# Performance work log

Hardware: AMD Instinct MI355X
Metric: run time of the kernel (lower is better)

The kernel has to match this reference:

```python
import jax, jax.numpy as jnp
import numpy as np

PC_RANGE = (-51.2, -51.2, -5.0, 51.2, 51.2, 3.0)
IMG_H, IMG_W = 256.0, 704.0
EPS = 1e-5


def conv2d(x, w, b, pad):
    y = jax.lax.conv_general_dilated(x, w, (1, 1), ((pad, pad), (pad, pad)),
                                     dimension_numbers=('NCHW', 'OIHW', 'NCHW'))
    return y + b[None, :, None, None]


def bilinear_sample(feat, grid):
    # torch.F.grid_sample, bilinear, zeros padding, align_corners=False
    # feat (BN,C,H,W), grid (BN,Q,D,2) in [-1,1] -> (BN,C,Q,D)
    BN, C, H, W = feat.shape
    ix = (grid[..., 0] + 1.0) * (W * 0.5) - 0.5
    iy = (grid[..., 1] + 1.0) * (H * 0.5) - 0.5
    x0 = jnp.floor(ix); y0 = jnp.floor(iy)
    x1 = x0 + 1.0; y1 = y0 + 1.0
    wx1 = ix - x0; wx0 = 1.0 - wx1
    wy1 = iy - y0; wy0 = 1.0 - wy1

    def corner(f, xi, yi):
        inb = ((xi >= 0) & (xi < W) & (yi >= 0) & (yi < H)).astype(f.dtype)
        xc = jnp.clip(xi, 0, W - 1).astype(jnp.int32)
        yc = jnp.clip(yi, 0, H - 1).astype(jnp.int32)
        idx = (yc * W + xc).reshape(-1)
        v = f.reshape(C, H * W)[:, idx].reshape((C,) + xi.shape)
        return v * inb[None]

    def sample_one(f, x0b, y0b, x1b, y1b, w00, w01, w10, w11):
        return (corner(f, x0b, y0b) * w00[None] + corner(f, x1b, y0b) * w01[None]
                + corner(f, x0b, y1b) * w10[None] + corner(f, x1b, y1b) * w11[None])

    return jax.vmap(sample_one)(feat, x0, y0, x1, y1,
                                wx0 * wy0, wx1 * wy0, wx0 * wy1, wx1 * wy1)


def ihr_forward(feat, bev_queries, bev_pos, reference_points, lidar2img, img_aug,
                w_pos, b_pos, w_attn, b_attn, w_out, b_out,
                conv_w, conv_b, bn_gamma, bn_beta, bn_mean, bn_var,
                se_w, se_b, cbam_w, cbam_b, bev_h, bev_w):
    B, Q, C = bev_queries.shape
    N = lidar2img.shape[1]
    q = bev_queries + bev_pos
    off = q @ w_pos + b_pos                                   # (B,Q,1) height offset
    # only_use_height: z <- sigmoid(inverse_sigmoid(z) + off)
    z = jnp.clip(reference_points[..., 2:3], 0.0, 1.0)
    z = jnp.log(jnp.clip(z, EPS, None) / jnp.clip(1.0 - z, EPS, None))
    z = jax.nn.sigmoid(z + off[:, None])                      # (B,D,Q,1)
    rp = jnp.concatenate([reference_points[..., :2], z], -1)  # updated ref points

    # --- feature_sampling ---
    xyz = jnp.stack([
        rp[..., 0] * (PC_RANGE[3] - PC_RANGE[0]) + PC_RANGE[0],
        rp[..., 1] * (PC_RANGE[4] - PC_RANGE[1]) + PC_RANGE[1],
        rp[..., 2] * (PC_RANGE[5] - PC_RANGE[2]) + PC_RANGE[2]], -1)  # (B,D,Q,3)
    pts = jnp.concatenate([xyz, jnp.ones_like(xyz[..., :1])], -1)
    pts = jnp.transpose(pts, (1, 0, 2, 3))                    # (D,B,Q,4)
    D = pts.shape[0]
    cam = jnp.einsum('bnij,dbqj->dbnqi', lidar2img, pts)       # (D,B,N,Q,3)
    depth = cam[..., 2:3]
    mask = depth > EPS
    cam4 = jnp.concatenate([cam[..., :2] / jnp.maximum(depth, EPS), depth,
                            jnp.ones_like(depth)], -1)
    cam2 = jnp.einsum('bnij,dbnqj->dbnqi', img_aug, cam4)[..., :2]
    cam2 = cam2 / jnp.array([IMG_W, IMG_H], cam2.dtype)
    cam2 = (cam2 - 0.5) * 2.0
    mask = (mask & (cam2[..., 0:1] > -1.0) & (cam2[..., 0:1] < 1.0)
            & (cam2[..., 1:2] > -1.0) & (cam2[..., 1:2] < 1.0))
    bev_mask = jnp.nan_to_num(jnp.transpose(mask, (1, 4, 3, 2, 0)).astype(feat.dtype))  # (B,1,Q,N,D)
    grid = jnp.transpose(cam2, (1, 2, 3, 0, 4)).reshape(B * N, Q, D, 2)
    samp = bilinear_sample(feat, grid)                         # (BN,C,Q,D)
    samp = samp.reshape(B, N, C, Q, D).transpose(0, 2, 3, 1, 4)  # (B,C,Q,N,D)
    samp = jnp.nan_to_num(samp)

    attn = jax.nn.sigmoid(q @ w_attn + b_attn).reshape(B, 1, Q, N, 1) * bev_mask
    out = (samp * attn).sum(axis=(3, 4))                       # (B,C,Q)  (D==1)
    out = out.transpose(0, 2, 1) @ w_out + b_out + bev_queries  # (B,Q,C)

    # --- vtransform: Conv3x3 -> BN(eval) -> ReLU -> SE -> CBAM(spatial) ---
    x = out.transpose(0, 2, 1).reshape(B, C, bev_h, bev_w)
    x = conv2d(x, conv_w, conv_b, 1)
    inv = jax.lax.rsqrt(bn_var + 1e-5)
    x = bn_gamma[None, :, None, None] * (x - bn_mean[None, :, None, None]) * inv[None, :, None, None] + bn_beta[None, :, None, None]
    x = jax.nn.relu(x)
    s = jax.nn.sigmoid(x.mean(axis=(2, 3)) @ se_w + se_b)      # SE: GAP + 1x1 conv
    x = x * s[:, :, None, None]
    mx = x.max(axis=1, keepdims=True)
    av = x.mean(axis=1, keepdims=True)
    a = jax.nn.sigmoid(conv2d(jnp.concatenate([mx, av], 1), cbam_w, cbam_b, 3))
    x = x * a
    out = x.reshape(B, C, bev_h * bev_w).transpose(0, 2, 1)
    return out, rp


def setup_inputs() -> dict:
    key = jax.random.key(0)
    ks = jax.random.split(key, 16)
    B, N, C, Q, D = 1, 6, 256, 128 * 128, 1
    H, W = 32, 88
    return {
        'feat': jax.random.normal(ks[0], (B * N, C, H, W), jnp.float32),
        'bev_queries': jax.random.normal(ks[1], (B, Q, C), jnp.float32),
        'bev_pos': jax.random.normal(ks[2], (B, Q, C), jnp.float32),
        'reference_points': jax.random.uniform(ks[3], (B, D, Q, 3), jnp.float32),
        'lidar2img': jax.random.normal(ks[4], (B, N, 3, 4), jnp.float32),
        'img_aug': jax.random.normal(ks[5], (B, N, 3, 4), jnp.float32),
        'w_pos': jax.random.normal(ks[6], (C, 1), jnp.float32) * 0.02,
        'b_pos': jnp.zeros((1,), jnp.float32),
        'w_attn': jax.random.normal(ks[7], (C, N), jnp.float32) * 0.02,
        'b_attn': jnp.zeros((N,), jnp.float32),
        'w_out': jax.random.normal(ks[8], (C, C), jnp.float32) * 0.02,
        'b_out': jnp.zeros((C,), jnp.float32),
        'conv_w': jax.random.normal(ks[9], (C, C, 3, 3), jnp.float32) * 0.02,
        'conv_b': jnp.zeros((C,), jnp.float32),
        'bn_gamma': jnp.ones((C,), jnp.float32),
        'bn_beta': jnp.zeros((C,), jnp.float32),
        'bn_mean': jnp.zeros((C,), jnp.float32),
        'bn_var': jax.random.uniform(ks[10], (C,), jnp.float32, 0.5, 1.5),
        'se_w': jax.random.normal(ks[11], (C, C), jnp.float32) * 0.02,
        'se_b': jnp.zeros((C,), jnp.float32),
        'cbam_w': jax.random.normal(ks[12], (1, 2, 7, 7), jnp.float32) * 0.1,
        'cbam_b': jnp.zeros((1,), jnp.float32),
        'bev_h': 128,
        'bev_w': 128,
    }


def reference(feat, bev_queries, bev_pos, reference_points, lidar2img, img_aug,
              w_pos, b_pos, w_attn, b_attn, w_out, b_out,
              conv_w, conv_b, bn_gamma, bn_beta, bn_mean, bn_var,
              se_w, se_b, cbam_w, cbam_b, bev_h, bev_w):
    return ihr_forward(feat, bev_queries, bev_pos, reference_points, lidar2img, img_aug,
                       w_pos, b_pos, w_attn, b_attn, w_out, b_out,
                       conv_w, conv_b, bn_gamma, bn_beta, bn_mean, bn_var,
                       se_w, se_b, cbam_w, cbam_b, bev_h, bev_w)
```

## Files before the change

### kernel.cpp

```cpp
#include <hip/hip_runtime.h>

typedef float  f32x4 __attribute__((ext_vector_type(4)));
typedef short  s16x8 __attribute__((ext_vector_type(8)));
typedef short  s16x4 __attribute__((ext_vector_type(4)));

__device__ __forceinline__ float bf2f(short h) {
    union { unsigned u; float f; } v; v.u = ((unsigned)(unsigned short)h) << 16; return v.f;
}
__device__ __forceinline__ short f2bf(float f) {
    union { float f; unsigned u; } v; v.f = f;
    unsigned r = v.u + 0x7FFFu + ((v.u >> 16) & 1u);
    return (short)(r >> 16);
}
__device__ __forceinline__ float sigf(float x) { return 1.f / (1.f + __expf(-x)); }


__global__ __launch_bounds__(256) void k_prep(
    const float* __restrict__ feat, const float* __restrict__ w_out,
    const float* __restrict__ conv_w, short* __restrict__ featT,
    short* __restrict__ woT, short* __restrict__ w9,
    short* __restrict__ Xp, float* __restrict__ chan_sums)
{
    __shared__ float tile[64][65];
    int b = blockIdx.x, t = threadIdx.x;
    if (b < 2340) {
        ((f32x4*)Xp)[b * 256 + t] = (f32x4){0.f, 0.f, 0.f, 0.f};
    } else if (b < 3396) {
        int bb = b - 2340;
        int n = bb / 176, r = bb % 176, ct = r / 44, ht = r % 44;
        int ty = t >> 6, tx = t & 63;
        const float* src = feat + (n * 256 + ct * 64) * 2816 + ht * 64;
        #pragma unroll
        for (int i = 0; i < 16; ++i) {
            int cl = ty * 16 + i;
            tile[cl][tx] = src[cl * 2816 + tx];
        }
        __syncthreads();
        short* dst = featT + (n * 2816 + ht * 64) * 256 + ct * 64;
        #pragma unroll
        for (int i = 0; i < 16; ++i) {
            int row = ty * 16 + i;
            dst[row * 256 + tx] = f2bf(tile[tx][row]);
        }
    } else if (b < 3652) {
        int idx = (b - 3396) * 256 + t;
        int j = idx >> 8, c = idx & 255;
        woT[j * 256 + c] = f2bf(w_out[c * 256 + j]);
    } else if (b < 3908) {
        int oc = (b - 3652) * 256 + t;
        const float* src = conv_w + oc * 9;
        #pragma unroll
        for (int k = 0; k < 9; ++k) w9[k * 65536 + oc] = f2bf(src[k]);
    } else {
        if (t < 256) chan_sums[t] = 0.f;
    }
}

__global__ __launch_bounds__(256) void k_sample(
    const float* __restrict__ bev_q, const float* __restrict__ bev_pos,
    const float* __restrict__ refp, const float* __restrict__ l2i,
    const float* __restrict__ aug, const float* __restrict__ w_pos,
    const float* __restrict__ b_pos, const float* __restrict__ w_attn,
    const float* __restrict__ b_attn, const short* __restrict__ featT,
    short* __restrict__ S, float* __restrict__ rp_out)
{
    int lane = threadIdx.x & 63;
    int qi = blockIdx.x * 4 + (threadIdx.x >> 6);

    f32x4 qv = *(const f32x4*)(bev_q + qi * 256 + lane * 4);
    {
        f32x4 pv = *(const f32x4*)(bev_pos + qi * 256 + lane * 4);
        qv[0] += pv[0]; qv[1] += pv[1]; qv[2] += pv[2]; qv[3] += pv[3];
    }
    f32x4 wp = *(const f32x4*)(w_pos + lane * 4);
    float op = qv[0]*wp[0] + qv[1]*wp[1] + qv[2]*wp[2] + qv[3]*wp[3];

    float la[6] = {0.f,0.f,0.f,0.f,0.f,0.f};
    const float* wa = w_attn + lane * 24;
    #pragma unroll
    for (int i = 0; i < 4; ++i) {
        #pragma unroll
        for (int n = 0; n < 6; ++n) la[n] += qv[i] * wa[i * 6 + n];
    }
    #pragma unroll
    for (int m = 1; m < 64; m <<= 1) {
        op += __shfl_xor(op, m);
        #pragma unroll
        for (int n = 0; n < 6; ++n) la[n] += __shfl_xor(la[n], m);
    }
    float off = op + b_pos[0];
    float attn[6];
    #pragma unroll
    for (int n = 0; n < 6; ++n) attn[n] = sigf(la[n] + b_attn[n]);

    float rx = refp[qi * 3 + 0], ry = refp[qi * 3 + 1], rz = refp[qi * 3 + 2];
    float zc = fminf(fmaxf(rz, 0.f), 1.f);
    float lg = logf(fmaxf(zc, 1e-5f) / fmaxf(1.f - zc, 1e-5f));
    float zn = sigf(lg + off);
    if (lane == 0) {
        rp_out[qi * 3 + 0] = rx;
        rp_out[qi * 3 + 1] = ry;
        rp_out[qi * 3 + 2] = zn;
    }

    float X = rx * 102.4f - 51.2f;
    float Yc = ry * 102.4f - 51.2f;
    float Z = zn * 8.f - 5.f;

    f32x4 acc = {0.f, 0.f, 0.f, 0.f};
    auto corner = [&](int n, int xi, int yi, float w) {
        if (xi >= 0 && xi < 88 && yi >= 0 && yi < 32) {
            s16x4 v = *(const s16x4*)(featT + (((n * 32 + yi) * 88 + xi) << 8) + (lane << 2));
            acc[0] += w * bf2f(v[0]); acc[1] += w * bf2f(v[1]);
            acc[2] += w * bf2f(v[2]); acc[3] += w * bf2f(v[3]);
        }
    };
    for (int n = 0; n < 6; ++n) {
        const float* L = l2i + n * 12;
        float cx = L[0]*X + L[1]*Yc + L[2]*Z  + L[3];
        float cy = L[4]*X + L[5]*Yc + L[6]*Z  + L[7];
        float d  = L[8]*X + L[9]*Yc + L[10]*Z + L[11];
        float dd = fmaxf(d, 1e-5f);
        float ux = cx / dd, uy = cy / dd;
        const float* A = aug + n * 12;
        float ax = A[0]*ux + A[1]*uy + A[2]*d + A[3];
        float ay = A[4]*ux + A[5]*uy + A[6]*d + A[7];
        float gx = (ax * (1.f / 704.f) - 0.5f) * 2.f;
        float gy = (ay * (1.f / 256.f) - 0.5f) * 2.f;
        bool m = (d > 1e-5f) && (gx > -1.f) && (gx < 1.f) && (gy > -1.f) && (gy < 1.f);
        if (m) {
            float ix = (gx + 1.f) * 44.f - 0.5f;
            float iy = (gy + 1.f) * 16.f - 0.5f;
            float x0f = floorf(ix), y0f = floorf(iy);
            float wx1 = ix - x0f, wx0 = 1.f - wx1;
            float wy1 = iy - y0f, wy0 = 1.f - wy1;
            int x0 = (int)x0f, y0 = (int)y0f, x1 = x0 + 1, y1 = y0 + 1;
            float wn = attn[n];
            corner(n, x0, y0, wn * wx0 * wy0);
            corner(n, x1, y0, wn * wx1 * wy0);
            corner(n, x0, y1, wn * wx0 * wy1);
            corner(n, x1, y1, wn * wx1 * wy1);
        }
    }
    s16x4 sv;
    sv[0] = f2bf(acc[0]); sv[1] = f2bf(acc[1]);
    sv[2] = f2bf(acc[2]); sv[3] = f2bf(acc[3]);
    *(s16x4*)(S + qi * 256 + lane * 4) = sv;
}

__global__ __launch_bounds__(256) void k_gemm(
    const short* __restrict__ S, const short* __restrict__ woT,
    const float* __restrict__ b_out, const float* __restrict__ bev_q,
    short* __restrict__ Xp)
{
    int tid = threadIdx.x, wave = tid >> 6, lane = tid & 63;
    int l15 = lane & 15, quad = lane >> 4;
    int p0 = blockIdx.x * 64, n0 = wave * 64;
    f32x4 acc[4][4];
    #pragma unroll
    for (int mt = 0; mt < 4; ++mt)
        #pragma unroll
        for (int nt = 0; nt < 4; ++nt) acc[mt][nt] = (f32x4){0.f,0.f,0.f,0.f};

    const short* Ab = S   + (p0 + l15) * 256 + quad * 8;
    const short* Bb = woT + (n0 + l15) * 256 + quad * 8;
    #pragma unroll
    for (int kb = 0; kb < 8; ++kb) {
        s16x8 a[4], b[4];
        #pragma unroll
        for (int mt = 0; mt < 4; ++mt) a[mt] = *(const s16x8*)(Ab + mt * 4096 + kb * 32);
        #pragma unroll
        for (int nt = 0; nt < 4; ++nt) b[nt] = *(const s16x8*)(Bb + nt * 4096 + kb * 32);
        #pragma unroll
        for (int mt = 0; mt < 4; ++mt)
            #pragma unroll
            for (int nt = 0; nt < 4; ++nt)
                acc[mt][nt] = __builtin_amdgcn_mfma_f32_16x16x32_bf16(a[mt], b[nt], acc[mt][nt], 0, 0, 0);
    }
    #pragma unroll
    for (int nt = 0; nt < 4; ++nt) {
        int j = n0 + nt * 16 + l15;
        float bo = b_out[j];
        #pragma unroll
        for (int mt = 0; mt < 4; ++mt) {
            #pragma unroll
            for (int r = 0; r < 4; ++r) {
                int p = p0 + mt * 16 + quad * 4 + r;
                float v = acc[mt][nt][r] + bo + bev_q[p * 256 + j];
                int h = p >> 7, w = p & 127;
                Xp[((h + 1) * 144 + (w + 1)) * 256 + j] = f2bf(v);
            }
        }
    }
}

__global__ __launch_bounds__(256) void k_conv(
    const short* __restrict__ Xp, const short* __restrict__ w9,
    const float* __restrict__ conv_b, const float* __restrict__ gamma,
    const float* __restrict__ beta, const float* __restrict__ mean,
    const float* __restrict__ var, short* __restrict__ Y)
{
    int tid = threadIdx.x, wave = tid >> 6, lane = tid & 63;
    int l15 = lane & 15, quad = lane >> 4;
    int p0 = blockIdx.x * 64;
    int h = p0 >> 7, w0 = p0 & 127;
    int m0 = wave * 64;
    f32x4 acc[4][4];
    #pragma unroll
    for (int mt = 0; mt < 4; ++mt)
        #pragma unroll
        for (int nt = 0; nt < 4; ++nt) acc[mt][nt] = (f32x4){0.f,0.f,0.f,0.f};

    const short* Ab0 = w9 + (m0 + l15) * 256 + quad * 8;
    for (int kh = 0; kh < 3; ++kh) {
        for (int kw = 0; kw < 3; ++kw) {
            const short* Ab = Ab0 + (kh * 3 + kw) * 65536;
            const short* Bb = Xp + ((h + kh) * 144 + (w0 + kw + l15)) * 256 + quad * 8;
            #pragma unroll
            for (int kb = 0; kb < 8; ++kb) {
                s16x8 a[4], b[4];
                #pragma unroll
                for (int mt = 0; mt < 4; ++mt) a[mt] = *(const s16x8*)(Ab + mt * 4096 + kb * 32);
                #pragma unroll
                for (int nt = 0; nt < 4; ++nt) b[nt] = *(const s16x8*)(Bb + nt * 4096 + kb * 32);
                #pragma unroll
                for (int mt = 0; mt < 4; ++mt)
                    #pragma unroll
                    for (int nt = 0; nt < 4; ++nt)
                        acc[mt][nt] = __builtin_amdgcn_mfma_f32_16x16x32_bf16(a[mt], b[nt], acc[mt][nt], 0, 0, 0);
            }
        }
    }
    #pragma unroll
    for (int mt = 0; mt < 4; ++mt) {
        #pragma unroll
        for (int r = 0; r < 4; ++r) {
            int o = m0 + mt * 16 + quad * 4 + r;
            float cb = conv_b[o], g = gamma[o], be = beta[o], mu = mean[o];
            float inv = rsqrtf(var[o] + 1e-5f);
            #pragma unroll
            for (int nt = 0; nt < 4; ++nt) {
                int p = p0 + nt * 16 + l15;
                float v = acc[mt][nt][r] + cb;
                v = g * (v - mu) * inv + be;
                v = fmaxf(v, 0.f);
                Y[p * 256 + o] = f2bf(v);
            }
        }
    }
}

__global__ __launch_bounds__(256) void k_csum(const short* __restrict__ Y, float* __restrict__ chan_sums)
{
    int c = threadIdx.x, p0 = blockIdx.x * 64;
    float s = 0.f;
    for (int i = 0; i < 64; ++i) s += bf2f(Y[(p0 + i) * 256 + c]);
    atomicAdd(chan_sums + c, s);
}

__global__ __launch_bounds__(256) void k_se(
    const float* __restrict__ chan_sums, const float* __restrict__ se_w,
    const float* __restrict__ se_b, float* __restrict__ sbuf)
{
    __shared__ float m[256];
    int t = threadIdx.x;
    m[t] = chan_sums[t] * (1.f / 16384.f);
    __syncthreads();
    float a = 0.f;
    for (int c = 0; c < 256; ++c) a += m[c] * se_w[c * 256 + t];
    sbuf[t] = sigf(a + se_b[t]);
}

__global__ __launch_bounds__(256) void k_mxav(
    const short* __restrict__ Y, const float* __restrict__ sbuf,
    float* __restrict__ mx, float* __restrict__ av)
{
    int lane = threadIdx.x & 63;
    int p = blockIdx.x * 4 + (threadIdx.x >> 6);
    f32x4 sv = *(const f32x4*)(sbuf + lane * 4);
    s16x4 yv = *(const s16x4*)(Y + p * 256 + lane * 4);
    float v0 = bf2f(yv[0]) * sv[0], v1 = bf2f(yv[1]) * sv[1];
    float v2 = bf2f(yv[2]) * sv[2], v3 = bf2f(yv[3]) * sv[3];
    float mval = fmaxf(fmaxf(v0, v1), fmaxf(v2, v3));
    float aval = v0 + v1 + v2 + v3;
    #pragma unroll
    for (int m = 1; m < 64; m <<= 1) {
        mval = fmaxf(mval, __shfl_xor(mval, m));
        aval += __shfl_xor(aval, m);
    }
    if (lane == 0) { mx[p] = mval; av[p] = aval * (1.f / 256.f); }
}

__global__ __launch_bounds__(256) void k_cbam(
    const float* __restrict__ mx, const float* __restrict__ av,
    const float* __restrict__ cw, const float* __restrict__ cb,
    float* __restrict__ amap)
{
    int p = blockIdx.x * 256 + threadIdx.x;
    int h = p >> 7, w = p & 127;
    float acc = cb[0];
    for (int kh = 0; kh < 7; ++kh) {
        int yy = h + kh - 3;
        if ((unsigned)yy >= 128u) continue;
        for (int kw = 0; kw < 7; ++kw) {
            int xx = w + kw - 3;
            if ((unsigned)xx >= 128u) continue;
            int q = yy * 128 + xx;
            acc += cw[kh * 7 + kw] * mx[q] + cw[49 + kh * 7 + kw] * av[q];
        }
    }
    amap[p] = sigf(acc);
}

__global__ __launch_bounds__(256) void k_final(
    const short* __restrict__ Y, const float* __restrict__ sbuf,
    const float* __restrict__ amap, float* __restrict__ out0)
{
    int lane = threadIdx.x & 63;
    int p = blockIdx.x * 4 + (threadIdx.x >> 6);
    float a = amap[p];
    f32x4 sv = *(const f32x4*)(sbuf + lane * 4);
    s16x4 yv = *(const s16x4*)(Y + p * 256 + lane * 4);
    f32x4 o;
    o[0] = bf2f(yv[0]) * sv[0] * a;
    o[1] = bf2f(yv[1]) * sv[1] * a;
    o[2] = bf2f(yv[2]) * sv[2] * a;
    o[3] = bf2f(yv[3]) * sv[3] * a;
    *(f32x4*)(out0 + p * 256 + lane * 4) = o;
}

extern "C" void kernel_launch(void* const* d_in, const int* in_sizes, int n_in,
                              void* d_out, int out_size, void* d_ws, size_t ws_size,
                              hipStream_t stream) {
    const float* feat     = (const float*)d_in[0];
    const float* bev_q    = (const float*)d_in[1];
    const float* bev_pos  = (const float*)d_in[2];
    const float* refp     = (const float*)d_in[3];
    const float* l2i      = (const float*)d_in[4];
    const float* aug      = (const float*)d_in[5];
    const float* w_pos    = (const float*)d_in[6];
    const float* b_pos    = (const float*)d_in[7];
    const float* w_attn   = (const float*)d_in[8];
    const float* b_attn   = (const float*)d_in[9];
    const float* w_out    = (const float*)d_in[10];
    const float* b_out    = (const float*)d_in[11];
    const float* conv_w   = (const float*)d_in[12];
    const float* conv_b   = (const float*)d_in[13];
    const float* bn_g     = (const float*)d_in[14];
    const float* bn_b     = (const float*)d_in[15];
    const float* bn_m     = (const float*)d_in[16];
    const float* bn_v     = (const float*)d_in[17];
    const float* se_w     = (const float*)d_in[18];
    const float* se_b     = (const float*)d_in[19];
    const float* cbam_w   = (const float*)d_in[20];
    const float* cbam_b   = (const float*)d_in[21];

    char* ws = (char*)d_ws;
    short* featT     = (short*)(ws + 0);
    short* Ybuf      = (short*)(ws + 0);
    short* Sbuf      = (short*)(ws + 8650752);
    short* Xp        = (short*)(ws + 17039360);
    short* w9        = (short*)(ws + 26624000);
    short* woT       = (short*)(ws + 27803648);
    float* chan_sums = (float*)(ws + 27934720);
    float* sbuf      = (float*)(ws + 27935744);
    float* mx        = (float*)(ws + 27936768);
    float* av        = (float*)(ws + 28002304);
    float* amap      = (float*)(ws + 28067840);

    float* out0   = (float*)d_out;
    float* rp_out = out0 + 16384 * 256;

    hipLaunchKernelGGL(k_prep, dim3(3909), dim3(256), 0, stream,
                       feat, w_out, conv_w, featT, woT, w9, Xp, chan_sums);
    hipLaunchKernelGGL(k_sample, dim3(4096), dim3(256), 0, stream,
                       bev_q, bev_pos, refp, l2i, aug, w_pos, b_pos, w_attn, b_attn,
                       featT, Sbuf, rp_out);
    hipLaunchKernelGGL(k_gemm, dim3(256), dim3(256), 0, stream,
                       Sbuf, woT, b_out, bev_q, Xp);
    hipLaunchKernelGGL(k_conv, dim3(256), dim3(256), 0, stream,
                       Xp, w9, conv_b, bn_g, bn_b, bn_m, bn_v, Ybuf);
    hipLaunchKernelGGL(k_csum, dim3(256), dim3(256), 0, stream, Ybuf, chan_sums);
    hipLaunchKernelGGL(k_se, dim3(1), dim3(256), 0, stream, chan_sums, se_w, se_b, sbuf);
    hipLaunchKernelGGL(k_mxav, dim3(4096), dim3(256), 0, stream, Ybuf, sbuf, mx, av);
    hipLaunchKernelGGL(k_cbam, dim3(64), dim3(256), 0, stream, mx, av, cbam_w, cbam_b, amap);
    hipLaunchKernelGGL(k_final, dim3(4096), dim3(256), 0, stream, Ybuf, sbuf, amap, out0);
}
```

Measured before the change: 274.7 us.

## Stage conv tiles in LDS via global_load_lds and split output channels across blocks

The 3x3 conv kernel used to read weight and activation fragments straight from global memory into registers, one 256-output-channel tile per block. It now copies 64x64 weight and pixel tiles into shared memory with async global-to-LDS loads, then runs MFMA from LDS. Each block now handles only a quarter of the output channels, giving 1024 blocks of 128 threads instead of 256 blocks. This adds parallelism and coalesced loads, but adds two barriers per K-chunk with no double buffering, and each activation tile is now loaded four times (once per channel quarter).

```diff
diff --git a/kernel.cpp b/kernel.cpp
--- a/kernel.cpp
+++ b/kernel.cpp
@@ -13,6 +13,13 @@
     return (short)(r >> 16);
 }
 __device__ __forceinline__ float sigf(float x) { return 1.f / (1.f + __expf(-x)); }
+
+__device__ __forceinline__ void gll16(const void* g, void* l) {
+    __builtin_amdgcn_global_load_lds(
+        (const __attribute__((address_space(1))) unsigned int*)(uintptr_t)g,
+        (__attribute__((address_space(3))) unsigned int*)(uintptr_t)l,
+        16, 0, 0);
+}
 
 
 __global__ __launch_bounds__(256) void k_prep(
@@ -194,57 +201,79 @@
     }
 }
 
-__global__ __launch_bounds__(256) void k_conv(
+__global__ __launch_bounds__(128) void k_conv(
     const short* __restrict__ Xp, const short* __restrict__ w9,
     const float* __restrict__ conv_b, const float* __restrict__ gamma,
     const float* __restrict__ beta, const float* __restrict__ mean,
     const float* __restrict__ var, short* __restrict__ Y)
 {
+    __shared__ short lA[4096];
+    __shared__ short lB[4096];
+
     int tid = threadIdx.x, wave = tid >> 6, lane = tid & 63;
     int l15 = lane & 15, quad = lane >> 4;
-    int p0 = blockIdx.x * 64;
+    int pxt = blockIdx.x >> 2, ocq = blockIdx.x & 3;
+    int p0 = pxt * 64;
     int h = p0 >> 7, w0 = p0 & 127;
-    int m0 = wave * 64;
-    f32x4 acc[4][4];
-    #pragma unroll
-    for (int mt = 0; mt < 4; ++mt)
+    int ocb = ocq * 64;
+
+    f32x4 acc[2][4];
+    #pragma unroll
+    for (int mt = 0; mt < 2; ++mt)
         #pragma unroll
         for (int nt = 0; nt < 4; ++nt) acc[mt][nt] = (f32x4){0.f,0.f,0.f,0.f};
 
-    const short* Ab0 = w9 + (m0 + l15) * 256 + quad * 8;
     for (int kh = 0; kh < 3; ++kh) {
         for (int kw = 0; kw < 3; ++kw) {
-            const short* Ab = Ab0 + (kh * 3 + kw) * 65536;
-            const short* Bb = Xp + ((h + kh) * 144 + (w0 + kw + l15)) * 256 + quad * 8;
-            #pragma unroll
-            for (int kb = 0; kb < 8; ++kb) {
-                s16x8 a[4], b[4];
+            const short* wsrc = w9 + ((kh * 3 + kw) << 16) + (ocb << 8);
+            const short* xsrc = Xp + ((h + kh) * 144 + (w0 + kw)) * 256;
+            for (int cb = 0; cb < 4; ++cb) {
+                int c0 = cb << 6;
                 #pragma unroll
-                for (int mt = 0; mt < 4; ++mt) a[mt] = *(const s16x8*)(Ab + mt * 4096 + kb * 32);
+                for (int j = 0; j < 4; ++j) {
+                    int ia = wave * 256 + j * 64 + lane;
+                    int cg = ia >> 6, ocl = ia & 63;
+                    gll16(wsrc + ocl * 256 + c0 + cg * 8, &lA[ia * 8]);
+                }
                 #pragma unroll
-                for (int nt = 0; nt < 4; ++nt) b[nt] = *(const s16x8*)(Bb + nt * 4096 + kb * 32);
+                for (int j = 0; j < 4; ++j) {
+                    int ib = wave * 256 + j * 64 + lane;
+                    int cg = ib >> 6, px = ib & 63;
+                    gll16(xsrc + px * 256 + c0 + cg * 8, &lB[ib * 8]);
+                }
+                __syncthreads();
                 #pragma unroll
-                for (int mt = 0; mt < 4; ++mt)
+                for (int s = 0; s < 2; ++s) {
+                    int cg = s * 4 + quad;
+                    s16x8 a[2], b[4];
+                    a[0] = *(const s16x8*)&lA[cg * 512 + (wave * 32 + l15) * 8];
+                    a[1] = *(const s16x8*)&lA[cg * 512 + (wave * 32 + 16 + l15) * 8];
                     #pragma unroll
                     for (int nt = 0; nt < 4; ++nt)
-                        acc[mt][nt] = __builtin_amdgcn_mfma_f32_16x16x32_bf16(a[mt], b[nt], acc[mt][nt], 0, 0, 0);
+                        b[nt] = *(const s16x8*)&lB[cg * 512 + (nt * 16 + l15) * 8];
+                    #pragma unroll
+                    for (int mt = 0; mt < 2; ++mt)
+                        #pragma unroll
+                        for (int nt = 0; nt < 4; ++nt)
+                            acc[mt][nt] = __builtin_amdgcn_mfma_f32_16x16x32_bf16(a[mt], b[nt], acc[mt][nt], 0, 0, 0);
+                }
+                __syncthreads();
             }
         }
     }
     #pragma unroll
-    for (int mt = 0; mt < 4; ++mt) {
+    for (int mt = 0; mt < 2; ++mt) {
         #pragma unroll
         for (int r = 0; r < 4; ++r) {
-            int o = m0 + mt * 16 + quad * 4 + r;
-            float cb = conv_b[o], g = gamma[o], be = beta[o], mu = mean[o];
+            int o = ocb + wave * 32 + mt * 16 + quad * 4 + r;
+            float cb_ = conv_b[o], g = gamma[o], be = beta[o], mu = mean[o];
             float inv = rsqrtf(var[o] + 1e-5f);
             #pragma unroll
             for (int nt = 0; nt < 4; ++nt) {
                 int p = p0 + nt * 16 + l15;
-                float v = acc[mt][nt][r] + cb;
+                float v = acc[mt][nt][r] + cb_;
                 v = g * (v - mu) * inv + be;
-                v = fmaxf(v, 0.f);
-                Y[p * 256 + o] = f2bf(v);
+                Y[p * 256 + o] = f2bf(fmaxf(v, 0.f));
             }
         }
     }
@@ -378,7 +407,7 @@
                        featT, Sbuf, rp_out);
     hipLaunchKernelGGL(k_gemm, dim3(256), dim3(256), 0, stream,
                        Sbuf, woT, b_out, bev_q, Xp);
-    hipLaunchKernelGGL(k_conv, dim3(256), dim3(256), 0, stream,
+    hipLaunchKernelGGL(k_conv, dim3(1024), dim3(128), 0, stream,
                        Xp, w9, conv_b, bn_g, bn_b, bn_m, bn_v, Ybuf);
     hipLaunchKernelGGL(k_csum, dim3(256), dim3(256), 0, stream, Ybuf, chan_sums);
     hipLaunchKernelGGL(k_se, dim3(1), dim3(256), 0, stream, chan_sums, se_w, se_b, sbuf);
```

Measured after the change: 278.0 us. No clear change (+1.2%).

## Stage conv tiles through LDS with double-buffered global_load_lds and 128x128 blocking

Applied to the files above, without the earlier changes.

The 3x3 implicit-GEMM conv kernel now has each block compute 128 output channels by one full 128-pixel row. Weight and input chunks of 64 channels are staged into LDS using direct global-to-LDS loads, double-buffered across 36 tap and channel steps. Until now every wave read its A and B fragments straight from global memory with no sharing between waves. The aim is to cut redundant global traffic and overlap loads with MFMA work, at the cost of a barrier each step, 64KB of LDS per block and a different block-to-row mapping.

```diff
diff --git a/kernel.cpp b/kernel.cpp
--- a/kernel.cpp
+++ b/kernel.cpp
@@ -13,6 +13,13 @@
     return (short)(r >> 16);
 }
 __device__ __forceinline__ float sigf(float x) { return 1.f / (1.f + __expf(-x)); }
+
+__device__ __forceinline__ void gll16(const void* g, void* l) {
+    __builtin_amdgcn_global_load_lds(
+        (const __attribute__((address_space(1))) unsigned int*)(uintptr_t)g,
+        (__attribute__((address_space(3))) unsigned int*)(uintptr_t)l,
+        16, 0, 0);
+}
 
 
 __global__ __launch_bounds__(256) void k_prep(
@@ -200,51 +207,76 @@
     const float* __restrict__ beta, const float* __restrict__ mean,
     const float* __restrict__ var, short* __restrict__ Y)
 {
+    __shared__ short lds[32768];
+
     int tid = threadIdx.x, wave = tid >> 6, lane = tid & 63;
     int l15 = lane & 15, quad = lane >> 4;
-    int p0 = blockIdx.x * 64;
-    int h = p0 >> 7, w0 = p0 & 127;
-    int m0 = wave * 64;
+    int sg = lane >> 3, cg = lane & 7;
+    int b = blockIdx.x;
+    int och = (b >> 3) & 1;
+    int h = (b & 7) * 16 + (b >> 4);
+    int mi = wave & 1, ni = wave >> 1;
+
     f32x4 acc[4][4];
     #pragma unroll
     for (int mt = 0; mt < 4; ++mt)
         #pragma unroll
         for (int nt = 0; nt < 4; ++nt) acc[mt][nt] = (f32x4){0.f,0.f,0.f,0.f};
 
-    const short* Ab0 = w9 + (m0 + l15) * 256 + quad * 8;
-    for (int kh = 0; kh < 3; ++kh) {
-        for (int kw = 0; kw < 3; ++kw) {
-            const short* Ab = Ab0 + (kh * 3 + kw) * 65536;
-            const short* Bb = Xp + ((h + kh) * 144 + (w0 + kw + l15)) * 256 + quad * 8;
-            #pragma unroll
-            for (int kb = 0; kb < 8; ++kb) {
-                s16x8 a[4], b[4];
+    auto stage = [&](int t) {
+        int tap = t >> 2, cb = t & 3;
+        int kh = tap / 3, kw = tap % 3;
+        int c0 = cb << 6;
+        const short* wsrc = w9 + (tap << 16) + (och << 15) + c0 + cg * 8;
+        const short* xsrc = Xp + ((h + kh) * 144 + kw) * 256 + c0 + cg * 8;
+        short* la = &lds[(t & 1) << 14];
+        short* lb = la + 8192;
+        #pragma unroll
+        for (int j = 0; j < 4; ++j) {
+            int row = j * 32 + wave * 8 + sg;
+            int slot = (j * 256 + wave * 64 + lane) * 8;
+            gll16(wsrc + row * 256, &la[slot]);
+            gll16(xsrc + row * 256, &lb[slot]);
+        }
+    };
+
+    stage(0);
+    for (int t = 0; t < 36; ++t) {
+        asm volatile("s_waitcnt vmcnt(0)\n\ts_barrier" ::: "memory");
+        if (t < 35) stage(t + 1);
+        const short* la = &lds[(t & 1) << 14];
+        const short* lb = la + 8192;
+        #pragma unroll
+        for (int s = 0; s < 2; ++s) {
+            int cgk = s * 4 + quad;
+            s16x8 af[4], bf[4];
+            #pragma unroll
+            for (int mt = 0; mt < 4; ++mt)
+                af[mt] = *(const s16x8*)&la[((mi * 64 + mt * 16 + l15) * 8 + cgk) * 8];
+            #pragma unroll
+            for (int nt = 0; nt < 4; ++nt)
+                bf[nt] = *(const s16x8*)&lb[((ni * 64 + nt * 16 + l15) * 8 + cgk) * 8];
+            #pragma unroll
+            for (int mt = 0; mt < 4; ++mt)
                 #pragma unroll
-                for (int mt = 0; mt < 4; ++mt) a[mt] = *(const s16x8*)(Ab + mt * 4096 + kb * 32);
-                #pragma unroll
-                for (int nt = 0; nt < 4; ++nt) b[nt] = *(const s16x8*)(Bb + nt * 4096 + kb * 32);
-                #pragma unroll
-                for (int mt = 0; mt < 4; ++mt)
-                    #pragma unroll
-                    for (int nt = 0; nt < 4; ++nt)
-                        acc[mt][nt] = __builtin_amdgcn_mfma_f32_16x16x32_bf16(a[mt], b[nt], acc[mt][nt], 0, 0, 0);
-            }
-        }
-    }
+                for (int nt = 0; nt < 4; ++nt)
+                    acc[mt][nt] = __builtin_amdgcn_mfma_f32_16x16x32_bf16(af[mt], bf[nt], acc[mt][nt], 0, 0, 0);
+        }
+    }
+
     #pragma unroll
     for (int mt = 0; mt < 4; ++mt) {
         #pragma unroll
         for (int r = 0; r < 4; ++r) {
-            int o = m0 + mt * 16 + quad * 4 + r;
-            float cb = conv_b[o], g = gamma[o], be = beta[o], mu = mean[o];
+            int o = (och << 7) + mi * 64 + mt * 16 + quad * 4 + r;
+            float cb_ = conv_b[o], g = gamma[o], be = beta[o], mu = mean[o];
             float inv = rsqrtf(var[o] + 1e-5f);
             #pragma unroll
             for (int nt = 0; nt < 4; ++nt) {
-                int p = p0 + nt * 16 + l15;
-                float v = acc[mt][nt][r] + cb;
+                int p = h * 128 + ni * 64 + nt * 16 + l15;
+                float v = acc[mt][nt][r] + cb_;
                 v = g * (v - mu) * inv + be;
-                v = fmaxf(v, 0.f);
-                Y[p * 256 + o] = f2bf(v);
+                Y[p * 256 + o] = f2bf(fmaxf(v, 0.f));
             }
         }
     }
```

Result: faster. 244.3 us (-11.1%).
